# Kernel tuning notes

Measured on AMD Instinct MI355X. Metric: run time of the kernel, lower is better.

Reference implementation:

```python
import jax, jax.numpy as jnp
import numpy as np

B, CIN, COUT, K = 8, 16, 32, 3
D = H = W = 64
NUM_W = CIN * COUT * K ** 3  # 13824
NUM_P = NUM_W + COUT         # 13856


def setup_inputs() -> dict:
    key = jax.random.key(0)
    ks = jax.random.split(key, 10)
    stdv = 1.0 / np.sqrt(CIN * K ** 3)
    return {
        "x": jax.random.normal(ks[0], (B, CIN, D, H, W), jnp.float32),
        "features": jax.random.normal(ks[1], (B, 10), jnp.float32),
        "fc0_w": jax.random.normal(ks[2], (16, 10), jnp.float32) * 0.3,
        "fc0_b": jax.random.normal(ks[3], (16,), jnp.float32) * 0.1,
        "a0": jnp.full((1,), 0.25, jnp.float32),
        "fc1_w": jax.random.normal(ks[4], (8, 16), jnp.float32) * 0.25,
        "fc1_b": jax.random.normal(ks[5], (8,), jnp.float32) * 0.1,
        "a1": jnp.full((1,), 0.25, jnp.float32),
        "wg_w": jax.random.uniform(ks[6], (NUM_P, 8), jnp.float32, -stdv, stdv),
        "wg_b": jax.random.uniform(ks[7], (NUM_P,), jnp.float32, -stdv / 100, stdv / 100),
    }


def _prelu(x, a):
    return jnp.where(x >= 0, x, a * x)


def reference(x, features, fc0_w, fc0_b, a0, fc1_w, fc1_b, a1, wg_w, wg_b):
    # hypernet MLP: [B,10] -> [B,16] -> [B,8] -> [B,NUM_P]
    h = _prelu(features @ fc0_w.T + fc0_b, a0)
    h = _prelu(h @ fc1_w.T + fc1_b, a1)
    params = h @ wg_w.T + wg_b  # [B, NUM_P]
    weights = params[:, :NUM_W].reshape(B, COUT, CIN, K, K, K)
    biases = params[:, NUM_W:]  # [B, COUT]

    def conv_one(xi, wi, bi):
        # xi: [CIN,D,H,W], wi: [COUT,CIN,K,K,K], bi: [COUT]
        y = jax.lax.conv_general_dilated(
            xi[None], wi, window_strides=(1, 1, 1),
            padding=[(1, 1)] * 3,
            dimension_numbers=("NCDHW", "OIDHW", "NCDHW"))
        return y[0] + bi[:, None, None, None]

    return jax.vmap(conv_one)(x, weights, biases)  # [B,COUT,D,H,W]
```

## Files before the change

kernel.cpp:

```cpp
#include <hip/hip_runtime.h>

typedef short short8 __attribute__((ext_vector_type(8)));
typedef float floatx4 __attribute__((ext_vector_type(4)));

#define BB   8
#define CIN  16
#define COUT 32
#define DD   64
#define NUM_W (CIN * COUT * 27)
#define NUM_P (NUM_W + COUT)
#define KPAD  448


__device__ __forceinline__ short f2bf(float f) {
    union { float f; unsigned u; } v; v.f = f;
    unsigned r = v.u + 0x7FFF + ((v.u >> 16) & 1);
    return (short)(r >> 16);
}

__device__ __forceinline__ unsigned pack2bf(float lo, float hi) {
    union { float f; unsigned u; } a, b; a.f = lo; b.f = hi;
    unsigned ra = a.u + 0x7FFF + ((a.u >> 16) & 1);
    unsigned rb = b.u + 0x7FFF + ((b.u >> 16) & 1);
    return (ra >> 16) | (rb & 0xFFFF0000u);
}

__device__ __forceinline__ int swz(int byte) {
    return byte ^ (((byte >> 7) & 7) << 4);
}

__global__ void hyper_kernel(const float* __restrict__ features,
                             const float* __restrict__ fc0_w,
                             const float* __restrict__ fc0_b,
                             const float* __restrict__ a0,
                             const float* __restrict__ fc1_w,
                             const float* __restrict__ fc1_b,
                             const float* __restrict__ a1,
                             const float* __restrict__ wg_w,
                             const float* __restrict__ wg_b,
                             float* __restrict__ h1out,
                             float* __restrict__ biasout) {
    __shared__ float h0[8][16];
    __shared__ float h1s[8][8];
    const int t = threadIdx.x;
    if (t < 128) {
        const int b = t >> 4, i = t & 15;
        float s = fc0_b[i];
        #pragma unroll
        for (int j = 0; j < 10; ++j) s += features[b * 10 + j] * fc0_w[i * 10 + j];
        const float a = a0[0];
        h0[b][i] = (s >= 0.f) ? s : a * s;
    }
    __syncthreads();
    if (t < 64) {
        const int b = t >> 3, i = t & 7;
        float s = fc1_b[i];
        #pragma unroll
        for (int j = 0; j < 16; ++j) s += h0[b][j] * fc1_w[i * 16 + j];
        const float a = a1[0];
        const float r = (s >= 0.f) ? s : a * s;
        h1s[b][i] = r;
        h1out[b * 8 + i] = r;
    }
    __syncthreads();
    {
        const int b = t >> 5, co = t & 31;
        const int p = NUM_W + co;
        float s = wg_b[p];
        #pragma unroll
        for (int j = 0; j < 8; ++j) s += h1s[b][j] * wg_w[p * 8 + j];
        biasout[b * 32 + co] = s;
    }
}

__global__ void wgen_kernel(const float* __restrict__ h1,
                            const float* __restrict__ wg_w,
                            const float* __restrict__ wg_b,
                            short* __restrict__ A) {
    const int b  = blockIdx.y;
    const int id = blockIdx.x * 256 + threadIdx.x;
    const int tap  = id % 28;
    const int rest = id / 28;
    const int ci   = rest & 15;
    const int co   = rest >> 4;
    float val = 0.f;
    if (tap < 27) {
        const int p = co * 432 + ci * 27 + tap;
        float s = wg_b[p];
        #pragma unroll
        for (int j = 0; j < 8; ++j) s += h1[b * 8 + j] * wg_w[p * 8 + j];
        val = s;
    }
    A[(b * 32 + co) * KPAD + tap * 16 + ci] = f2bf(val);
}

__device__ __forceinline__ void stage_one(const float* __restrict__ x, char* xsb,
                                          int b, int cp, int w4,
                                          int dz, int phys, int zd, int zh) {
    float4 v0 = {0.f, 0.f, 0.f, 0.f};
    float4 v1 = {0.f, 0.f, 0.f, 0.f};
    if (zd >= 0 && zd < DD && zh >= 0 && zh < DD) {
        const size_t gbase =
            (((size_t)(b * CIN + 2 * cp) * DD + zd) * DD + zh) * DD + w4;
        v0 = *(const float4*)(x + gbase);
        v1 = *(const float4*)(x + gbase + (size_t)DD * DD * DD);
    }
    const int rb = ((dz * 6 + phys) * 66 + (w4 + 1)) * 32 + 4 * cp;
    *(unsigned*)(xsb + swz(rb))      = pack2bf(v0.x, v1.x);
    *(unsigned*)(xsb + swz(rb + 32)) = pack2bf(v0.y, v1.y);
    *(unsigned*)(xsb + swz(rb + 64)) = pack2bf(v0.z, v1.z);
    *(unsigned*)(xsb + swz(rb + 96)) = pack2bf(v0.w, v1.w);
}

__global__ __launch_bounds__(256, 2) void conv_mfma_kernel(
        const float* __restrict__ x,
        const short* __restrict__ A,
        const float* __restrict__ bias,
        float* __restrict__ out) {
    __shared__ uint4 xs4[2376];
    __shared__ uint4 als4[1664];
    char* xsb = (char*)xs4;
    char* alb = (char*)als4;

    const int t    = threadIdx.x;
    const int lane = t & 63;
    const int wave = t >> 6;
    const int n16  = lane & 15;
    const int q    = lane >> 4;

    const int lin   = blockIdx.x;
    const int o     = (lin & 7) * 128 + (lin >> 3);
    const int b     = o >> 7;
    const int rest  = o & 127;
    const int d     = rest >> 1;
    const int hbase = (rest & 1) * 32;

    const short* Ab = A + (size_t)(b * 32) * KPAD;

    #pragma unroll
    for (int i = 0; i < 7; ++i) {
        const int u = t + i * 256;
        if (u < 1664) {
            const int cm = u >> 6;
            const int c  = cm >> 1, mt = cm & 1;
            const int nn = (u >> 2) & 15, qs = u & 3;
            als4[u] = *(const uint4*)(Ab + (mt * 16 + nn) * KPAD + c * 32 + qs * 8);
        }
    }

    short8 af13[2];
    af13[0] = *(const short8*)(Ab + n16 * KPAD + 13 * 32 + q * 8);
    af13[1] = *(const short8*)(Ab + (16 + n16) * KPAD + 13 * 32 + q * 8);

    if (t < 72) {
        const int rowl = t >> 2;
        const int wz   = ((t >> 1) & 1) * 65;
        const int half = t & 1;
        const uint4 z4 = {0u, 0u, 0u, 0u};
        *(uint4*)(xsb + swz((rowl * 66 + wz) * 32 + half * 16)) = z4;
    }

    const float bv0 = bias[b * 32 + n16];
    const float bv1 = bias[b * 32 + 16 + n16];

    const int tid16 = wave * 4 + q;
    const int cp    = tid16 & 7;
    const int rhalf = tid16 >> 3;
    const int w4    = n16 * 4;

    const int ci_base2 = (q & 1) * 16;
    const int qh       = q >> 1;
    const int aoff     = n16 * 64 + q * 16;

    #pragma unroll 1
    for (int it = 0; it < 8; ++it) {
        const int h0 = hbase + it * 4;
        const int p  = h0 % 6;

        __syncthreads();

        if (it == 0) {
            #pragma unroll
            for (int i = 0; i < 9; ++i) {
                const int rowl = rhalf * 9 + i;
                const int dz = rowl / 6, hz = rowl % 6;
                int phys = p + hz; if (phys >= 6) phys -= 6;
                stage_one(x, xsb, b, cp, w4, dz, phys, d + dz - 1, h0 + hz - 1);
            }
        } else {
            #pragma unroll
            for (int i = 0; i < 6; ++i) {
                const int idx = rhalf * 6 + i;
                const int dz = idx >> 2, j = idx & 3;
                int phys = p + 2 + j; if (phys >= 6) phys -= 6;
                stage_one(x, xsb, b, cp, w4, dz, phys, d + dz - 1, h0 + 1 + j);
            }
        }
        __syncthreads();

        floatx4 acc[2][4];
        #pragma unroll
        for (int mt = 0; mt < 2; ++mt)
            #pragma unroll
            for (int nt = 0; nt < 4; ++nt) acc[mt][nt] = (floatx4){0.f, 0.f, 0.f, 0.f};

        __builtin_amdgcn_s_setprio(1);
        #pragma unroll
        for (int c = 0; c < 14; ++c) {
            int tap = 2 * c + qh;
            if (tap > 26) tap = 26;
            const int kd = tap / 9;
            const int r  = tap - kd * 9;
            const int kh = r / 3;
            const int kw = r - kh * 3;
            int prow = p + wave + kh; if (prow >= 6) prow -= 6;
            const int rowb = ((kd * 6 + prow) * 66 + kw) * 32 + ci_base2;
            const short8 a0 = (c < 13) ? *(const short8*)(alb + (c * 2) * 1024 + aoff)
                                       : af13[0];
            const short8 a1 = (c < 13) ? *(const short8*)(alb + (c * 2 + 1) * 1024 + aoff)
                                       : af13[1];
            #pragma unroll
            for (int nt = 0; nt < 4; ++nt) {
                const short8 xf = *(const short8*)(xsb + swz(rowb + (nt * 16 + n16) * 32));
                acc[0][nt] = __builtin_amdgcn_mfma_f32_16x16x32_bf16(
                                 xf, a0, acc[0][nt], 0, 0, 0);
                acc[1][nt] = __builtin_amdgcn_mfma_f32_16x16x32_bf16(
                                 xf, a1, acc[1][nt], 0, 0, 0);
            }
        }
        __builtin_amdgcn_s_setprio(0);

        const int hh = h0 + wave;
        #pragma unroll
        for (int mt = 0; mt < 2; ++mt) {
            const float bv = mt ? bv1 : bv0;
            #pragma unroll
            for (int nt = 0; nt < 4; ++nt) {
                floatx4 rr = acc[mt][nt];
                rr[0] += bv; rr[1] += bv; rr[2] += bv; rr[3] += bv;
                *(floatx4*)(out + (((size_t)(b * COUT + mt * 16 + n16) * DD + d) * DD + hh) * DD
                                 + nt * 16 + q * 4) = rr;
            }
        }
    }
}

extern "C" void kernel_launch(void* const* d_in, const int* in_sizes, int n_in,
                              void* d_out, int out_size, void* d_ws, size_t ws_size,
                              hipStream_t stream) {
    const float* x        = (const float*)d_in[0];
    const float* features = (const float*)d_in[1];
    const float* fc0_w    = (const float*)d_in[2];
    const float* fc0_b    = (const float*)d_in[3];
    const float* a0       = (const float*)d_in[4];
    const float* fc1_w    = (const float*)d_in[5];
    const float* fc1_b    = (const float*)d_in[6];
    const float* a1       = (const float*)d_in[7];
    const float* wg_w     = (const float*)d_in[8];
    const float* wg_b     = (const float*)d_in[9];

    float* ws    = (float*)d_ws;
    float* h1    = ws;
    float* biasp = ws + 64;
    short* A     = (short*)(ws + 320);

    hyper_kernel<<<1, 256, 0, stream>>>(features, fc0_w, fc0_b, a0,
                                        fc1_w, fc1_b, a1, wg_w, wg_b, h1, biasp);
    wgen_kernel<<<dim3(56, BB), 256, 0, stream>>>(h1, wg_w, wg_b, A);
    conv_mfma_kernel<<<dim3(1024), 256, 0, stream>>>(x, A, biasp, (float*)d_out);
}
```

Before: 456.8 us.

## Emit weights in MFMA fragment order and batch global loads during staging

The weight generator now writes the bf16 weight matrix directly in the per-lane MFMA fragment layout. The conv kernel can then copy it into LDS with contiguous uint4 loads and fetch the tap-13 fragments with a simple lane-indexed load, with no strided gathers. The x staging loop is restructured to issue three rows of global loads before any LDS stores, which raises memory-level parallelism. The cost is higher register pressure, which matters under launch bounds of 2 blocks per CU.

Result: faster. 426.7 us (-6.6%).

```diff
diff --git a/kernel.cpp b/kernel.cpp
--- a/kernel.cpp
+++ b/kernel.cpp
@@ -9,7 +9,6 @@
 #define DD   64
 #define NUM_W (CIN * COUT * 27)
 #define NUM_P (NUM_W + COUT)
-#define KPAD  448
 
 
 __device__ __forceinline__ short f2bf(float f) {
@@ -91,25 +90,12 @@
         for (int j = 0; j < 8; ++j) s += h1[b * 8 + j] * wg_w[p * 8 + j];
         val = s;
     }
-    A[(b * 32 + co) * KPAD + tap * 16 + ci] = f2bf(val);
-}
-
-__device__ __forceinline__ void stage_one(const float* __restrict__ x, char* xsb,
-                                          int b, int cp, int w4,
-                                          int dz, int phys, int zd, int zh) {
-    float4 v0 = {0.f, 0.f, 0.f, 0.f};
-    float4 v1 = {0.f, 0.f, 0.f, 0.f};
-    if (zd >= 0 && zd < DD && zh >= 0 && zh < DD) {
-        const size_t gbase =
-            (((size_t)(b * CIN + 2 * cp) * DD + zd) * DD + zh) * DD + w4;
-        v0 = *(const float4*)(x + gbase);
-        v1 = *(const float4*)(x + gbase + (size_t)DD * DD * DD);
-    }
-    const int rb = ((dz * 6 + phys) * 66 + (w4 + 1)) * 32 + 4 * cp;
-    *(unsigned*)(xsb + swz(rb))      = pack2bf(v0.x, v1.x);
-    *(unsigned*)(xsb + swz(rb + 32)) = pack2bf(v0.y, v1.y);
-    *(unsigned*)(xsb + swz(rb + 64)) = pack2bf(v0.z, v1.z);
-    *(unsigned*)(xsb + swz(rb + 96)) = pack2bf(v0.w, v1.w);
+    const int c    = tap >> 1;
+    const int qs   = (tap & 1) * 2 + (ci >> 3);
+    const int nn   = co & 15;
+    const int mt   = co >> 4;
+    const int lane = qs * 16 + nn;
+    A[((((size_t)b * 14 + c) * 2 + mt) * 64 + lane) * 8 + (ci & 7)] = f2bf(val);
 }
 
 __global__ __launch_bounds__(256, 2) void conv_mfma_kernel(
@@ -135,22 +121,17 @@
     const int d     = rest >> 1;
     const int hbase = (rest & 1) * 32;
 
-    const short* Ab = A + (size_t)(b * 32) * KPAD;
+    const uint4* AFb = (const uint4*)A + (size_t)b * 1792;
 
     #pragma unroll
     for (int i = 0; i < 7; ++i) {
         const int u = t + i * 256;
-        if (u < 1664) {
-            const int cm = u >> 6;
-            const int c  = cm >> 1, mt = cm & 1;
-            const int nn = (u >> 2) & 15, qs = u & 3;
-            als4[u] = *(const uint4*)(Ab + (mt * 16 + nn) * KPAD + c * 32 + qs * 8);
-        }
+        if (u < 1664) als4[u] = AFb[u];
     }
 
     short8 af13[2];
-    af13[0] = *(const short8*)(Ab + n16 * KPAD + 13 * 32 + q * 8);
-    af13[1] = *(const short8*)(Ab + (16 + n16) * KPAD + 13 * 32 + q * 8);
+    af13[0] = *(const short8*)(AFb + 26 * 64 + lane);
+    af13[1] = *(const short8*)(AFb + 27 * 64 + lane);
 
     if (t < 72) {
         const int rowl = t >> 2;
@@ -170,7 +151,7 @@
 
     const int ci_base2 = (q & 1) * 16;
     const int qh       = q >> 1;
-    const int aoff     = n16 * 64 + q * 16;
+    const int aoff     = lane * 16;
 
     #pragma unroll 1
     for (int it = 0; it < 8; ++it) {
@@ -181,19 +162,63 @@
 
         if (it == 0) {
             #pragma unroll
-            for (int i = 0; i < 9; ++i) {
-                const int rowl = rhalf * 9 + i;
-                const int dz = rowl / 6, hz = rowl % 6;
-                int phys = p + hz; if (phys >= 6) phys -= 6;
-                stage_one(x, xsb, b, cp, w4, dz, phys, d + dz - 1, h0 + hz - 1);
+            for (int bt = 0; bt < 3; ++bt) {
+                float4 va[3], vb[3];
+                int rbs[3];
+                #pragma unroll
+                for (int j = 0; j < 3; ++j) {
+                    const int rowl = rhalf * 9 + bt * 3 + j;
+                    const int dz = rowl / 6, hz = rowl % 6;
+                    int phys = p + hz; if (phys >= 6) phys -= 6;
+                    const int zd = d + dz - 1, zh = h0 + hz - 1;
+                    va[j] = (float4){0.f, 0.f, 0.f, 0.f};
+                    vb[j] = (float4){0.f, 0.f, 0.f, 0.f};
+                    if (zd >= 0 && zd < DD && zh >= 0 && zh < DD) {
+                        const size_t gbase =
+                            (((size_t)(b * CIN + 2 * cp) * DD + zd) * DD + zh) * DD + w4;
+                        va[j] = *(const float4*)(x + gbase);
+                        vb[j] = *(const float4*)(x + gbase + (size_t)DD * DD * DD);
+                    }
+                    rbs[j] = ((dz * 6 + phys) * 66 + (w4 + 1)) * 32 + 4 * cp;
+                }
+                #pragma unroll
+                for (int j = 0; j < 3; ++j) {
+                    *(unsigned*)(xsb + swz(rbs[j]))      = pack2bf(va[j].x, vb[j].x);
+                    *(unsigned*)(xsb + swz(rbs[j] + 32)) = pack2bf(va[j].y, vb[j].y);
+                    *(unsigned*)(xsb + swz(rbs[j] + 64)) = pack2bf(va[j].z, vb[j].z);
+                    *(unsigned*)(xsb + swz(rbs[j] + 96)) = pack2bf(va[j].w, vb[j].w);
+                }
             }
         } else {
             #pragma unroll
-            for (int i = 0; i < 6; ++i) {
-                const int idx = rhalf * 6 + i;
-                const int dz = idx >> 2, j = idx & 3;
-                int phys = p + 2 + j; if (phys >= 6) phys -= 6;
-                stage_one(x, xsb, b, cp, w4, dz, phys, d + dz - 1, h0 + 1 + j);
+            for (int bt = 0; bt < 2; ++bt) {
+                float4 va[3], vb[3];
+                int rbs[3];
+                #pragma unroll
+                for (int j = 0; j < 3; ++j) {
+                    const int idx = rhalf * 6 + bt * 3 + j;
+                    const int dz = idx >> 2, jj = idx & 3;
+                    int phys = p + 2 + jj; if (phys >= 6) phys -= 6;
+                    const int zd = d + dz - 1, zh = h0 + 1 + jj;
+                    va[j] = (float4){0.f, 0.f, 0.f, 0.f};
+                    vb[j] = (float4){0.f, 0.f, 0.f, 0.f};
+                    if (zd >= 0 && zd < DD) {
+                        if (zh < DD) {
+                            const size_t gbase =
+                                (((size_t)(b * CIN + 2 * cp) * DD + zd) * DD + zh) * DD + w4;
+                            va[j] = *(const float4*)(x + gbase);
+                            vb[j] = *(const float4*)(x + gbase + (size_t)DD * DD * DD);
+                        }
+                    }
+                    rbs[j] = ((dz * 6 + phys) * 66 + (w4 + 1)) * 32 + 4 * cp;
+                }
+                #pragma unroll
+                for (int j = 0; j < 3; ++j) {
+                    *(unsigned*)(xsb + swz(rbs[j]))      = pack2bf(va[j].x, vb[j].x);
+                    *(unsigned*)(xsb + swz(rbs[j] + 32)) = pack2bf(va[j].y, vb[j].y);
+                    *(unsigned*)(xsb + swz(rbs[j] + 64)) = pack2bf(va[j].z, vb[j].z);
+                    *(unsigned*)(xsb + swz(rbs[j] + 96)) = pack2bf(va[j].w, vb[j].w);
+                }
             }
         }
         __syncthreads();
```
